# Kernel optimization log

Measured on AMD Instinct MI355X. Metric: run time of the kernel, lower is better.

Reference implementation:

```python
import jax, jax.numpy as jnp
import numpy as np


def setup_inputs() -> dict:
    key = jax.random.key(0)
    k1, k2 = jax.random.split(key)
    B, N, M = 32, 4096, 4096
    pred = jax.random.normal(k1, (B, N, 3), dtype=jnp.float32)
    target = jax.random.normal(k2, (B, M, 3), dtype=jnp.float32)
    return {"pred": pred, "target": target}


def reference(pred, target):
    # pairwise euclidean distances: [B, N, M]
    # d2 = |p|^2 + |t|^2 - 2 p.t  (matches torch.cdist p=2)
    p2 = jnp.sum(pred * pred, axis=-1)                      # [B, N]
    t2 = jnp.sum(target * target, axis=-1)                  # [B, M]
    pt = jnp.einsum('bnd,bmd->bnm', pred, target)           # [B, N, M]
    d2 = p2[:, :, None] + t2[:, None, :] - 2.0 * pt
    dist = jnp.sqrt(jnp.maximum(d2, 0.0))                   # [B, N, M]
    min_d = jnp.min(dist, axis=2)                           # [B, N]
    return jnp.mean(min_d)
```

## Files before the change

### kernel.cpp

```cpp
#include <hip/hip_runtime.h>


typedef short bf16x8 __attribute__((ext_vector_type(8)));
typedef float f32x16 __attribute__((ext_vector_type(16)));

constexpr int Bc = 32;
constexpr int Nc = 4096;
constexpr int Mc = 4096;
constexpr int BLOCK = 256;
constexpr int PTS = Bc * Nc;
constexpr int S = 8;
constexpr int TPB = 512;
constexpr int PPB = 512;

__device__ __forceinline__ unsigned short brne(float x) {
  unsigned u = __float_as_uint(x);
  return (unsigned short)((u + 0x7FFFu + ((u >> 16) & 1u)) >> 16);
}
__device__ __forceinline__ float bf2f(unsigned short h) {
  return __uint_as_float(((unsigned)h) << 16);
}
__device__ __forceinline__ unsigned pack(unsigned short lo, unsigned short hi) {
  return (unsigned)lo | ((unsigned)hi << 16);
}

__global__ __launch_bounds__(BLOCK)
void emd_main_kernel(const float* __restrict__ pred,
                     const float* __restrict__ target,
                     float* __restrict__ slices) {
  __shared__ uint4 lds[1024];

  const int pg = blockIdx.x >> 3;
  const int s = blockIdx.x & 7;
  const int b = pg >> 3;
  const int lane = threadIdx.x & 63;
  const int half = lane >> 5;
  const int l31 = lane & 31;
  const int wave = threadIdx.x >> 6;
  const unsigned short ONE = 0x3F80;

#pragma unroll
  for (int j = 0; j < 2; ++j) {
    const int p = threadIdx.x + j * BLOCK;
    const size_t gi = (size_t)pg * PPB + p;
    float x = pred[3 * gi], y = pred[3 * gi + 1], z = pred[3 * gi + 2];
    unsigned short xh = brne(x), xl = brne(x - bf2f(xh));
    unsigned short yh = brne(y), yl = brne(y - bf2f(yh));
    unsigned short zh = brne(z), zl = brne(z - bf2f(zh));
    float p2 = fmaf(x, x, fmaf(y, y, z * z));
    unsigned short ph = brne(p2), pl = brne(p2 - bf2f(ph));
    lds[p] = make_uint4(pack(xh, xl), pack(xh, yh), pack(yl, yh), pack(zh, zl));
    lds[512 + p] = make_uint4(pack(zh, ONE), pack(ONE, ph), pack(pl, 0), 0);
  }
  __syncthreads();

  bf16x8 bfr[4];
#pragma unroll
  for (int f = 0; f < 4; ++f) {
    uint4 u = lds[half * 512 + wave * 128 + f * 32 + l31];
    bfr[f] = *(const bf16x8*)&u;
  }
  __syncthreads();

  if (threadIdx.x < 128) {
    const size_t tbase = (size_t)b * Mc + s * TPB;
    const float4* tp4 = (const float4*)(target + tbase * 3);
    float4 f0 = tp4[3 * threadIdx.x + 0];
    float4 f1 = tp4[3 * threadIdx.x + 1];
    float4 f2 = tp4[3 * threadIdx.x + 2];
    float cx[4] = {f0.x, f0.w, f1.z, f2.y};
    float cy[4] = {f0.y, f1.x, f1.w, f2.z};
    float cz[4] = {f0.z, f1.y, f2.x, f2.w};
#pragma unroll
    for (int j = 0; j < 4; ++j) {
      const int pt = 4 * threadIdx.x + j;
      float X = -2.0f * cx[j], Y = -2.0f * cy[j], Z = -2.0f * cz[j];
      unsigned short Xh = brne(X), Xl = brne(X - bf2f(Xh));
      unsigned short Yh = brne(Y), Yl = brne(Y - bf2f(Yh));
      unsigned short Zh = brne(Z), Zl = brne(Z - bf2f(Zh));
      float t2 = 0.25f * fmaf(X, X, fmaf(Y, Y, Z * Z));
      unsigned short th = brne(t2), tl = brne(t2 - bf2f(th));
      lds[pt] =
          make_uint4(pack(Xh, Xh), pack(Xl, Yh), pack(Yh, Yl), pack(Zh, Zh));
      lds[512 + pt] =
          make_uint4(pack(Zl, th), pack(tl, ONE), pack(ONE, 0), 0);
    }
  }
  __syncthreads();

  float rA[4], rB[4];
#pragma unroll
  for (int f = 0; f < 4; ++f) { rA[f] = 3.4e38f; rB[f] = 3.4e38f; }

  const int abase = half * 512 + l31;
#pragma unroll 2
  for (int t = 0; t < 16; ++t) {
    uint4 au = lds[abase + t * 32];
    bf16x8 af = *(const bf16x8*)&au;
    f32x16 z{};
    f32x16 d0 = __builtin_amdgcn_mfma_f32_32x32x16_bf16(af, bfr[0], z, 0, 0, 0);
    f32x16 d1 = __builtin_amdgcn_mfma_f32_32x32x16_bf16(af, bfr[1], z, 0, 0, 0);
    f32x16 d2 = __builtin_amdgcn_mfma_f32_32x32x16_bf16(af, bfr[2], z, 0, 0, 0);
    f32x16 d3 = __builtin_amdgcn_mfma_f32_32x32x16_bf16(af, bfr[3], z, 0, 0, 0);
#pragma unroll
    for (int i = 0; i < 16; i += 4) {
      rA[0] = fminf(fminf(d0[i], d0[i + 1]), rA[0]);
      rB[0] = fminf(fminf(d0[i + 2], d0[i + 3]), rB[0]);
      rA[1] = fminf(fminf(d1[i], d1[i + 1]), rA[1]);
      rB[1] = fminf(fminf(d1[i + 2], d1[i + 3]), rB[1]);
      rA[2] = fminf(fminf(d2[i], d2[i + 1]), rA[2]);
      rB[2] = fminf(fminf(d2[i + 2], d2[i + 3]), rB[2]);
      rA[3] = fminf(fminf(d3[i], d3[i + 1]), rA[3]);
      rB[3] = fminf(fminf(d3[i + 2], d3[i + 3]), rB[3]);
    }
  }

  const size_t sbase = (size_t)s * PTS + (size_t)pg * PPB + wave * 128;
#pragma unroll
  for (int f = 0; f < 4; ++f) {
    float rr = fminf(rA[f], rB[f]);
    rr = fminf(rr, __shfl_xor(rr, 32, 64));
    if (lane < 32) slices[sbase + f * 32 + l31] = fmaxf(rr, 0.0f);
  }
}

__global__ __launch_bounds__(BLOCK) void emd_finish_kernel(
    const float4* __restrict__ slices, float* __restrict__ out) {
  __shared__ float wsum[4];
  const int i = blockIdx.x * BLOCK + threadIdx.x;
  float4 m = slices[i];
#pragma unroll
  for (int s = 1; s < S; ++s) {
    float4 v = slices[(size_t)s * (PTS / 4) + i];
    m.x = fminf(m.x, v.x);
    m.y = fminf(m.y, v.y);
    m.z = fminf(m.z, v.z);
    m.w = fminf(m.w, v.w);
  }
  float ss = sqrtf(m.x) + sqrtf(m.y) + sqrtf(m.z) + sqrtf(m.w);
#pragma unroll
  for (int off = 32; off > 0; off >>= 1) ss += __shfl_down(ss, off, 64);
  if ((threadIdx.x & 63) == 0) wsum[threadIdx.x >> 6] = ss;
  __syncthreads();
  if (threadIdx.x == 0) {
    float tot = (wsum[0] + wsum[1]) + (wsum[2] + wsum[3]);
    atomicAdd(out, tot * (1.0f / (float)PTS));
  }
}

extern "C" void kernel_launch(void* const* d_in, const int* in_sizes, int n_in,
                              void* d_out, int out_size, void* d_ws, size_t ws_size,
                              hipStream_t stream) {
  const float* pred = (const float*)d_in[0];
  const float* target = (const float*)d_in[1];
  float* out = (float*)d_out;
  float* slices = (float*)d_ws;

  emd_main_kernel<<<dim3((PTS / PPB) * S), dim3(BLOCK), 0, stream>>>(
      pred, target, slices);
  emd_finish_kernel<<<dim3(PTS / 4 / BLOCK), dim3(BLOCK), 0, stream>>>(
      (const float4*)slices, out);
}
```

Before: 85.42 us.

## Double pred points per block to reuse target tiles across more MFMAs

Each block now handles 1024 pred points instead of 512, so each wave holds 8 B-fragments and issues 8 MFMAs per target A-fragment load, halving target preprocessing and LDS A-loads per unit of work. Pred loading is vectorized with float4 reads, and the kernel is pinned to 4 waves per EU. The grid halves in size, which may reduce latency hiding and raises register pressure because of the 16 extra min accumulators.

```diff
diff --git a/kernel.cpp b/kernel.cpp
--- a/kernel.cpp
+++ b/kernel.cpp
@@ -11,7 +11,7 @@
 constexpr int PTS = Bc * Nc;
 constexpr int S = 8;
 constexpr int TPB = 512;
-constexpr int PPB = 512;
+constexpr int PPB = 1024;
 
 __device__ __forceinline__ unsigned short brne(float x) {
   unsigned u = __float_as_uint(x);
@@ -25,39 +25,50 @@
 }
 
 __global__ __launch_bounds__(BLOCK)
+__attribute__((amdgpu_waves_per_eu(4, 4)))
 void emd_main_kernel(const float* __restrict__ pred,
                      const float* __restrict__ target,
                      float* __restrict__ slices) {
-  __shared__ uint4 lds[1024];
+  __shared__ uint4 lds[2048];
 
   const int pg = blockIdx.x >> 3;
   const int s = blockIdx.x & 7;
-  const int b = pg >> 3;
+  const int b = pg >> 2;
   const int lane = threadIdx.x & 63;
   const int half = lane >> 5;
   const int l31 = lane & 31;
   const int wave = threadIdx.x >> 6;
   const unsigned short ONE = 0x3F80;
 
+  {
+    const float4* pp4 = (const float4*)(pred + (size_t)pg * PPB * 3);
+    float4 f0 = pp4[3 * threadIdx.x + 0];
+    float4 f1 = pp4[3 * threadIdx.x + 1];
+    float4 f2 = pp4[3 * threadIdx.x + 2];
+    float cx[4] = {f0.x, f0.w, f1.z, f2.y};
+    float cy[4] = {f0.y, f1.x, f1.w, f2.z};
+    float cz[4] = {f0.z, f1.y, f2.x, f2.w};
 #pragma unroll
-  for (int j = 0; j < 2; ++j) {
-    const int p = threadIdx.x + j * BLOCK;
-    const size_t gi = (size_t)pg * PPB + p;
-    float x = pred[3 * gi], y = pred[3 * gi + 1], z = pred[3 * gi + 2];
-    unsigned short xh = brne(x), xl = brne(x - bf2f(xh));
-    unsigned short yh = brne(y), yl = brne(y - bf2f(yh));
-    unsigned short zh = brne(z), zl = brne(z - bf2f(zh));
-    float p2 = fmaf(x, x, fmaf(y, y, z * z));
-    unsigned short ph = brne(p2), pl = brne(p2 - bf2f(ph));
-    lds[p] = make_uint4(pack(xh, xl), pack(xh, yh), pack(yl, yh), pack(zh, zl));
-    lds[512 + p] = make_uint4(pack(zh, ONE), pack(ONE, ph), pack(pl, 0), 0);
+    for (int j = 0; j < 4; ++j) {
+      const int p = 4 * threadIdx.x + j;
+      float x = cx[j], y = cy[j], z = cz[j];
+      unsigned short xh = brne(x), xl = brne(x - bf2f(xh));
+      unsigned short yh = brne(y), yl = brne(y - bf2f(yh));
+      unsigned short zh = brne(z), zl = brne(z - bf2f(zh));
+      float p2 = fmaf(x, x, fmaf(y, y, z * z));
+      unsigned short ph = brne(p2), pl = brne(p2 - bf2f(ph));
+      lds[p] =
+          make_uint4(pack(xh, xl), pack(xh, yh), pack(yl, yh), pack(zh, zl));
+      lds[1024 + p] =
+          make_uint4(pack(zh, ONE), pack(ONE, ph), pack(pl, 0), 0);
+    }
   }
   __syncthreads();
 
-  bf16x8 bfr[4];
+  bf16x8 bfr[8];
 #pragma unroll
-  for (int f = 0; f < 4; ++f) {
-    uint4 u = lds[half * 512 + wave * 128 + f * 32 + l31];
+  for (int f = 0; f < 8; ++f) {
+    uint4 u = lds[half * 1024 + wave * 256 + f * 32 + l31];
     bfr[f] = *(const bf16x8*)&u;
   }
   __syncthreads();
@@ -88,36 +99,55 @@
   }
   __syncthreads();
 
-  float rA[4], rB[4];
+  float rA[8], rB[8];
 #pragma unroll
-  for (int f = 0; f < 4; ++f) { rA[f] = 3.4e38f; rB[f] = 3.4e38f; }
+  for (int f = 0; f < 8; ++f) { rA[f] = 3.4e38f; rB[f] = 3.4e38f; }
 
+  const f32x16 zc{};
   const int abase = half * 512 + l31;
 #pragma unroll 2
   for (int t = 0; t < 16; ++t) {
     uint4 au = lds[abase + t * 32];
     bf16x8 af = *(const bf16x8*)&au;
-    f32x16 z{};
-    f32x16 d0 = __builtin_amdgcn_mfma_f32_32x32x16_bf16(af, bfr[0], z, 0, 0, 0);
-    f32x16 d1 = __builtin_amdgcn_mfma_f32_32x32x16_bf16(af, bfr[1], z, 0, 0, 0);
-    f32x16 d2 = __builtin_amdgcn_mfma_f32_32x32x16_bf16(af, bfr[2], z, 0, 0, 0);
-    f32x16 d3 = __builtin_amdgcn_mfma_f32_32x32x16_bf16(af, bfr[3], z, 0, 0, 0);
+    {
+      f32x16 d0 = __builtin_amdgcn_mfma_f32_32x32x16_bf16(af, bfr[0], zc, 0, 0, 0);
+      f32x16 d1 = __builtin_amdgcn_mfma_f32_32x32x16_bf16(af, bfr[1], zc, 0, 0, 0);
+      f32x16 d2 = __builtin_amdgcn_mfma_f32_32x32x16_bf16(af, bfr[2], zc, 0, 0, 0);
+      f32x16 d3 = __builtin_amdgcn_mfma_f32_32x32x16_bf16(af, bfr[3], zc, 0, 0, 0);
 #pragma unroll
-    for (int i = 0; i < 16; i += 4) {
-      rA[0] = fminf(fminf(d0[i], d0[i + 1]), rA[0]);
-      rB[0] = fminf(fminf(d0[i + 2], d0[i + 3]), rB[0]);
-      rA[1] = fminf(fminf(d1[i], d1[i + 1]), rA[1]);
-      rB[1] = fminf(fminf(d1[i + 2], d1[i + 3]), rB[1]);
-      rA[2] = fminf(fminf(d2[i], d2[i + 1]), rA[2]);
-      rB[2] = fminf(fminf(d2[i + 2], d2[i + 3]), rB[2]);
-      rA[3] = fminf(fminf(d3[i], d3[i + 1]), rA[3]);
-      rB[3] = fminf(fminf(d3[i + 2], d3[i + 3]), rB[3]);
+      for (int i = 0; i < 16; i += 4) {
+        rA[0] = fminf(fminf(d0[i], d0[i + 1]), rA[0]);
+        rB[0] = fminf(fminf(d0[i + 2], d0[i + 3]), rB[0]);
+        rA[1] = fminf(fminf(d1[i], d1[i + 1]), rA[1]);
+        rB[1] = fminf(fminf(d1[i + 2], d1[i + 3]), rB[1]);
+        rA[2] = fminf(fminf(d2[i], d2[i + 1]), rA[2]);
+        rB[2] = fminf(fminf(d2[i + 2], d2[i + 3]), rB[2]);
+        rA[3] = fminf(fminf(d3[i], d3[i + 1]), rA[3]);
+        rB[3] = fminf(fminf(d3[i + 2], d3[i + 3]), rB[3]);
+      }
+    }
+    {
+      f32x16 d0 = __builtin_amdgcn_mfma_f32_32x32x16_bf16(af, bfr[4], zc, 0, 0, 0);
+      f32x16 d1 = __builtin_amdgcn_mfma_f32_32x32x16_bf16(af, bfr[5], zc, 0, 0, 0);
+      f32x16 d2 = __builtin_amdgcn_mfma_f32_32x32x16_bf16(af, bfr[6], zc, 0, 0, 0);
+      f32x16 d3 = __builtin_amdgcn_mfma_f32_32x32x16_bf16(af, bfr[7], zc, 0, 0, 0);
+#pragma unroll
+      for (int i = 0; i < 16; i += 4) {
+        rA[4] = fminf(fminf(d0[i], d0[i + 1]), rA[4]);
+        rB[4] = fminf(fminf(d0[i + 2], d0[i + 3]), rB[4]);
+        rA[5] = fminf(fminf(d1[i], d1[i + 1]), rA[5]);
+        rB[5] = fminf(fminf(d1[i + 2], d1[i + 3]), rB[5]);
+        rA[6] = fminf(fminf(d2[i], d2[i + 1]), rA[6]);
+        rB[6] = fminf(fminf(d2[i + 2], d2[i + 3]), rB[6]);
+        rA[7] = fminf(fminf(d3[i], d3[i + 1]), rA[7]);
+        rB[7] = fminf(fminf(d3[i + 2], d3[i + 3]), rB[7]);
+      }
     }
   }
 
-  const size_t sbase = (size_t)s * PTS + (size_t)pg * PPB + wave * 128;
+  const size_t sbase = (size_t)s * PTS + (size_t)pg * PPB + wave * 256;
 #pragma unroll
-  for (int f = 0; f < 4; ++f) {
+  for (int f = 0; f < 8; ++f) {
     float rr = fminf(rA[f], rB[f]);
     rr = fminf(rr, __shfl_xor(rr, 32, 64));
     if (lane < 32) slices[sbase + f * 32 + l31] = fmaxf(rr, 0.0f);
```

Result: faster. 79.59 us (-6.8%).
